# Optimization experiments

Measured on AMD Instinct MI355X. Metric: run time of the kernel, lower is better.

The kernel has to match this reference:

```python
import jax, jax.numpy as jnp
import numpy as np

N_NODES = 100000
N_EDGES = 1600000
D_IN, D_HID, D_OUT = 128, 64, 16


def _glorot(key, shape):
    lim = float(np.sqrt(6.0 / (shape[0] + shape[1])))
    return jax.random.uniform(key, shape, jnp.float32, -lim, lim)


def setup_inputs() -> dict:
    key = jax.random.key(0)
    k1, k2, k3 = jax.random.split(key, 3)
    x = jax.random.normal(k1, (N_NODES, D_IN), dtype=jnp.float32)
    edge_index = jax.random.randint(k2, (2, N_EDGES), 0, N_NODES, dtype=jnp.int64)
    kw1, kw2 = jax.random.split(k3)
    W1 = _glorot(kw1, (D_IN, D_HID))
    b1 = jnp.zeros((D_HID,), jnp.float32)
    W2 = _glorot(kw2, (D_HID, D_OUT))
    b2 = jnp.zeros((D_OUT,), jnp.float32)
    return {"x": x, "edge_index": edge_index, "W1": W1, "b1": b1, "W2": W2, "b2": b2}


def _gcn_conv(h, W, b, src, dst, norm, n_nodes):
    # PyG GCNConv: linear first, then normalized neighbor aggregation, then bias.
    h = h @ W                                        # [N, d_out]
    msg = h[src] * norm[:, None]                     # gather over edges(+self loops)
    out = jax.ops.segment_sum(msg, dst, num_segments=n_nodes)  # scatter-add
    return out + b


def reference(x, edge_index, W1, b1, W2, b2):
    n = x.shape[0]
    loop = jnp.arange(n, dtype=edge_index.dtype)
    src = jnp.concatenate([edge_index[0], loop])     # add self loops
    dst = jnp.concatenate([edge_index[1], loop])
    # symmetric normalization D^-1/2 (A+I) D^-1/2
    deg = jax.ops.segment_sum(jnp.ones(src.shape[0], x.dtype), dst, num_segments=n)
    dinv = jnp.where(deg > 0, jax.lax.rsqrt(jnp.maximum(deg, 1e-12)), 0.0)
    norm = dinv[src] * dinv[dst]                     # [E+N]

    out = _gcn_conv(x, W1, b1, src, dst, norm, n)
    out = jax.nn.sigmoid(out)
    # dropout p=0.5 with training=False -> identity (eval mode)
    out = _gcn_conv(out, W2, b2, src, dst, norm, n)
    return jax.nn.log_softmax(out, axis=1)
```

## Files before the change

kernel.cpp:

```cpp
#include <hip/hip_runtime.h>
#include <hip/hip_bf16.h>


constexpr int D_IN  = 128;
constexpr int D_HID = 64;
constexpr int D_OUT = 16;

constexpr int WSHIFT  = 9;
constexpr int MAXB    = 256;
constexpr int BCAP    = 12288;
constexpr int CSRCAP  = 16384;
constexpr int BIN_CAP = 48;
constexpr int CHUNK   = 4096;

typedef __attribute__((ext_vector_type(8))) short bf16x8;
typedef __attribute__((ext_vector_type(4))) float f32x4;
typedef __attribute__((ext_vector_type(2))) float f32x2;

__device__ inline float bflo(unsigned u){ return __uint_as_float(u << 16); }
__device__ inline float bfhi(unsigned u){ return __uint_as_float(u & 0xffff0000u); }
__device__ inline unsigned f2bu(float f){
    __hip_bfloat16 h = __float2bfloat16(f);
    return (unsigned)*reinterpret_cast<unsigned short*>(&h);
}
__device__ inline float sigf(float x){ return 1.0f / (1.0f + __expf(-x)); }

__global__ __launch_bounds__(256) void k_bucketize(
    const int* __restrict__ ei, const unsigned* __restrict__ xraw,
    int* __restrict__ flags, unsigned* __restrict__ gcur,
    unsigned* __restrict__ gbuf, int ne, int B)
{
    __shared__ unsigned bcnt[MAXB];
    __shared__ unsigned bbase[MAXB];
    __shared__ unsigned bins[MAXB * BIN_CAP];
    __shared__ int s_i64;

    const int t = threadIdx.x, lane = t & 63, wv = t >> 6;
    const int e0 = blockIdx.x * CHUNK;

    if (t < MAXB) bcnt[t] = 0u;
    if (wv == 0){
        int w = ei[2 * lane + 1];
        unsigned long long m = __ballot(w == 0);
        if (lane == 0) s_i64 = (__popcll(m) > 48) ? 1 : 0;
        if (blockIdx.x == 0){
            unsigned u = xraw[lane];
            unsigned h0 = u & 0xffffu, h1 = u >> 16;
            unsigned ex0 = (h0 >> 7) & 0xffu, ex1 = (h1 >> 7) & 0xffu;
            bool bad0 = !((h0 & 0x7fffu) == 0 || (ex0 >= 97 && ex0 <= 157));
            bool bad1 = !((h1 & 0x7fffu) == 0 || (ex1 >= 97 && ex1 <= 157));
            unsigned long long m0 = __ballot(bad0);
            unsigned long long m1 = __ballot(bad1);
            if (lane == 0){
                int bad = __popcll(m0) + __popcll(m1);
                flags[0] = (bad > 8) ? 0 : 1;
                flags[1] = s_i64;
            }
        }
    }
    __syncthreads();
    const int i64 = s_i64;
    const bool vec = ((ne & 1) == 0);

    #pragma unroll
    for (int k = 0; k < CHUNK / 512; ++k){
        int e = e0 + k * 512 + 2 * t;
        int s0, d0, s1, d1;
        int cntE = 0;
        if (vec && e < ne){
            if (i64){
                int4 sp = *(const int4*)&ei[2 * e];
                int4 dp = *(const int4*)&ei[2 * (ne + e)];
                s0 = sp.x; s1 = sp.z; d0 = dp.x; d1 = dp.z;
            } else {
                int2 sp = *(const int2*)&ei[e];
                int2 dp = *(const int2*)&ei[ne + e];
                s0 = sp.x; s1 = sp.y; d0 = dp.x; d1 = dp.y;
            }
            cntE = 2;
        } else {
            if (e < ne){
                if (i64){ s0 = ei[2*e]; d0 = ei[2*(ne+e)]; }
                else    { s0 = ei[e];   d0 = ei[ne+e]; }
                cntE = 1;
                if (e + 1 < ne){
                    if (i64){ s1 = ei[2*(e+1)]; d1 = ei[2*(ne+e+1)]; }
                    else    { s1 = ei[e+1];     d1 = ei[ne+e+1]; }
                    cntE = 2;
                }
            }
        }
        #pragma unroll
        for (int j = 0; j < 2; ++j){
            if (j < cntE){
                int s = j ? s1 : s0, d = j ? d1 : d0;
                int b = d >> WSHIFT;
                unsigned v = ((unsigned)s << WSHIFT) | ((unsigned)d & ((1u << WSHIFT) - 1));
                unsigned p = atomicAdd(&bcnt[b], 1u);
                if (p < (unsigned)BIN_CAP){
                    bins[b * BIN_CAP + p] = v;
                } else {
                    unsigned g = atomicAdd(&gcur[b], 1u);
                    gbuf[(size_t)b * BCAP + g] = v;
                }
            }
        }
    }
    __syncthreads();

    if (t < B){
        unsigned c = min(bcnt[t], (unsigned)BIN_CAP);
        bbase[t] = atomicAdd(&gcur[t], c);
    }
    __syncthreads();

    for (int b = wv; b < B; b += 4){
        unsigned c = min(bcnt[b], (unsigned)BIN_CAP);
        unsigned ba = bbase[b];
        for (unsigned o = lane; o < c; o += 64)
            gbuf[(size_t)b * BCAP + ba + o] = bins[b * BIN_CAP + o];
    }
}

__global__ __launch_bounds__(1024) void k_build(
    const unsigned* __restrict__ gbuf, const unsigned* __restrict__ gcnt,
    unsigned* __restrict__ off, unsigned* __restrict__ offend,
    float* __restrict__ dinv, int* __restrict__ csr, int n, int B)
{
    __shared__ unsigned hist[512];
    __shared__ unsigned offl[512];
    __shared__ unsigned wsums[8];

    const int t = threadIdx.x, lane = t & 63, wv = t >> 6;
    const int b = blockIdx.x;
    const int base = b << WSHIFT;
    const int nodes = min(512, n - base);
    const unsigned bb = (unsigned)b * CSRCAP;

    if (t < 512) hist[t] = 0u;
    __syncthreads();
    const unsigned cnt = gcnt[b];
    const unsigned* mybuf = gbuf + (size_t)b * BCAP;

    for (unsigned i = t; i < cnt; i += 1024)
        atomicAdd(&hist[mybuf[i] & ((1u << WSHIFT) - 1)], 1u);
    __syncthreads();

    unsigned v = 0, p = 0, x = 0;
    if (t < 512){
        v = hist[t];
        p = (v + 7u) & ~7u;
        x = p;
        #pragma unroll
        for (int o = 1; o < 64; o <<= 1){
            unsigned y = __shfl_up(x, o, 64);
            if (lane >= o) x += y;
        }
        if (lane == 63) wsums[wv] = x;
    }
    __syncthreads();
    if (t == 0){
        unsigned run = 0;
        #pragma unroll
        for (int w = 0; w < 8; ++w){ unsigned tv = wsums[w]; wsums[w] = run; run += tv; }
    }
    __syncthreads();
    if (t < 512) offl[t] = x - p + wsums[wv];
    __syncthreads();

    if (t < nodes){
        off[base + t]    = bb + offl[t];
        offend[base + t] = bb + offl[t] + p;
        dinv[base + t]   = rsqrtf(1.0f + (float)v);
    }
    __syncthreads();

    if (t < 512) hist[t] = offl[t];
    __syncthreads();

    for (unsigned i = t; i < cnt; i += 1024){
        unsigned rec = mybuf[i];
        unsigned pos = atomicAdd(&hist[rec & ((1u << WSHIFT) - 1)], 1u);
        csr[bb + pos] = (int)(rec >> WSHIFT);
    }
    __syncthreads();

    if (t < nodes){
        unsigned s = offl[t] + v, e2 = offl[t] + p;
        for (unsigned j = s; j < e2; ++j) csr[bb + j] = n;
    }
}

__global__ __launch_bounds__(256) void k_linear1(
    const unsigned* __restrict__ xraw, const unsigned* __restrict__ w1raw,
    const int* __restrict__ flags, const float* __restrict__ dinv,
    unsigned char* __restrict__ h1f, int n)
{
    const int lane = threadIdx.x & 63;
    const int wv   = threadIdx.x >> 6;
    const int m = lane & 15, q = lane >> 4;
    const int isBf16 = flags[0];

    if (blockIdx.x == 0 && threadIdx.x < 16)
        ((unsigned*)(h1f + (size_t)n * 64))[threadIdx.x] = 0u;

    bf16x8 bfr[4][4];
    if (isBf16){
        const unsigned short* w = (const unsigned short*)w1raw;
        #pragma unroll
        for (int kc = 0; kc < 4; ++kc)
            #pragma unroll
            for (int ct = 0; ct < 4; ++ct)
                #pragma unroll
                for (int j = 0; j < 8; ++j)
                    bfr[kc][ct][j] = (short)w[(kc*32 + q*8 + j) * D_HID + ct*16 + m];
    } else {
        const float* w = (const float*)w1raw;
        #pragma unroll
        for (int kc = 0; kc < 4; ++kc)
            #pragma unroll
            for (int ct = 0; ct < 4; ++ct)
                #pragma unroll
                for (int j = 0; j < 8; ++j)
                    bfr[kc][ct][j] = (short)f2bu(w[(kc*32 + q*8 + j) * D_HID + ct*16 + m]);
    }

    const int ntiles = (n + 15) >> 4;
    for (int tile = blockIdx.x * 4 + wv; tile < ntiles; tile += gridDim.x * 4){
        const int node0 = tile << 4;
        int arow = node0 + m; if (arow >= n) arow = n - 1;
        f32x4 ac0 = {0,0,0,0}, ac1 = {0,0,0,0}, ac2 = {0,0,0,0}, ac3 = {0,0,0,0};
        #pragma unroll
        for (int kc = 0; kc < 4; ++kc){
            bf16x8 a;
            if (isBf16){
                uint4 u = *(const uint4*)((const unsigned short*)xraw + (size_t)arow * D_IN + kc*32 + q*8);
                a = *reinterpret_cast<bf16x8*>(&u);
            } else {
                const float* xp = (const float*)xraw + (size_t)arow * D_IN + kc*32 + q*8;
                float4 f0 = *(const float4*)xp;
                float4 f1 = *(const float4*)(xp + 4);
                a[0]=(short)f2bu(f0.x); a[1]=(short)f2bu(f0.y); a[2]=(short)f2bu(f0.z); a[3]=(short)f2bu(f0.w);
                a[4]=(short)f2bu(f1.x); a[5]=(short)f2bu(f1.y); a[6]=(short)f2bu(f1.z); a[7]=(short)f2bu(f1.w);
            }
            ac0 = __builtin_amdgcn_mfma_f32_16x16x32_bf16(a, bfr[kc][0], ac0, 0, 0, 0);
            ac1 = __builtin_amdgcn_mfma_f32_16x16x32_bf16(a, bfr[kc][1], ac1, 0, 0, 0);
            ac2 = __builtin_amdgcn_mfma_f32_16x16x32_bf16(a, bfr[kc][2], ac2, 0, 0, 0);
            ac3 = __builtin_amdgcn_mfma_f32_16x16x32_bf16(a, bfr[kc][3], ac3, 0, 0, 0);
        }
        #pragma unroll
        for (int i = 0; i < 4; ++i){
            int nr = node0 + q*4 + i;
            if (nr < n){
                float di = dinv[nr];
                int lo = __builtin_amdgcn_cvt_pk_fp8_f32(ac0[i] * di, ac1[i] * di, 0, false);
                int w4 = __builtin_amdgcn_cvt_pk_fp8_f32(ac2[i] * di, ac3[i] * di, lo, true);
                *(unsigned*)(h1f + (size_t)nr * 64 + m * 4) = (unsigned)w4;
            }
        }
    }
}

__global__ __launch_bounds__(256) void k_aggA(
    const unsigned* __restrict__ off, const unsigned* __restrict__ offend,
    const int* __restrict__ csr_src,
    const float* __restrict__ dinv, const unsigned char* __restrict__ h1f,
    const unsigned* __restrict__ b1raw, const unsigned* __restrict__ w2raw,
    const int* __restrict__ flags,
    unsigned short* __restrict__ h2s, int n)
{
    __shared__ unsigned short act_s[16][72];

    const int lane = threadIdx.x & 63;
    const int wv   = threadIdx.x >> 6;
    const int grp  = lane >> 4;
    const int f    = lane & 15;
    const int dl   = wv * 4 + grp;
    const int d    = blockIdx.x * 16 + dl;
    const int isBf16 = flags[0];

    bf16x8 w2f[2];
    if (wv == 0){
        const int m0 = lane & 15, q0 = lane >> 4;
        if (isBf16){
            const unsigned short* w = (const unsigned short*)w2raw;
            #pragma unroll
            for (int kc = 0; kc < 2; ++kc)
                #pragma unroll
                for (int j = 0; j < 8; ++j)
                    w2f[kc][j] = (short)w[(kc*32 + q0*8 + j) * D_OUT + m0];
        } else {
            const float* w = (const float*)w2raw;
            #pragma unroll
            for (int kc = 0; kc < 2; ++kc)
                #pragma unroll
                for (int j = 0; j < 8; ++j)
                    w2f[kc][j] = (short)f2bu(w[(kc*32 + q0*8 + j) * D_OUT + m0]);
        }
        if (blockIdx.x == 0 && lane < 4)
            ((uint2*)(h2s + (size_t)n * D_OUT))[lane] = make_uint2(0u, 0u);
    }

    if (d < n){
        const int beg = (int)off[d], end = (int)offend[d];
        float a0=0.f, a1=0.f, a2=0.f, a3=0.f;
        for (int i = beg; i < end; i += 8){
            uint4 cA = *(const uint4*)&csr_src[i];
            uint4 cB = *(const uint4*)&csr_src[i + 4];
            unsigned u0 = *(const unsigned*)&h1f[(size_t)(unsigned)cA.x * 64 + f * 4];
            unsigned u1 = *(const unsigned*)&h1f[(size_t)(unsigned)cA.y * 64 + f * 4];
            unsigned u2 = *(const unsigned*)&h1f[(size_t)(unsigned)cA.z * 64 + f * 4];
            unsigned u3 = *(const unsigned*)&h1f[(size_t)(unsigned)cA.w * 64 + f * 4];
            unsigned u4 = *(const unsigned*)&h1f[(size_t)(unsigned)cB.x * 64 + f * 4];
            unsigned u5 = *(const unsigned*)&h1f[(size_t)(unsigned)cB.y * 64 + f * 4];
            unsigned u6 = *(const unsigned*)&h1f[(size_t)(unsigned)cB.z * 64 + f * 4];
            unsigned u7 = *(const unsigned*)&h1f[(size_t)(unsigned)cB.w * 64 + f * 4];
            #pragma unroll
            for (int r = 0; r < 8; ++r){
                unsigned uu = r==0?u0: r==1?u1: r==2?u2: r==3?u3: r==4?u4: r==5?u5: r==6?u6: u7;
                f32x2 p01 = __builtin_amdgcn_cvt_pk_f32_fp8((int)uu, false);
                f32x2 p23 = __builtin_amdgcn_cvt_pk_f32_fp8((int)uu, true);
                a0 += p01.x; a1 += p01.y; a2 += p23.x; a3 += p23.y;
            }
        }
        {
            unsigned su = *(const unsigned*)&h1f[(size_t)d * 64 + f * 4];
            f32x2 p01 = __builtin_amdgcn_cvt_pk_f32_fp8((int)su, false);
            f32x2 p23 = __builtin_amdgcn_cvt_pk_f32_fp8((int)su, true);
            a0 += p01.x; a1 += p01.y; a2 += p23.x; a3 += p23.y;
        }
        const float dd = dinv[d];
        float b0, b1v, b2v, b3v;
        if (isBf16){
            const unsigned short* bs = (const unsigned short*)b1raw;
            b0  = bflo(bs[f]);      b1v = bflo(bs[f + 16]);
            b2v = bflo(bs[f + 32]); b3v = bflo(bs[f + 48]);
        } else {
            const float* bs = (const float*)b1raw;
            b0 = bs[f]; b1v = bs[f + 16]; b2v = bs[f + 32]; b3v = bs[f + 48];
        }
        act_s[dl][f]      = (unsigned short)f2bu(sigf(fmaf(a0, dd, b0)));
        act_s[dl][f + 16] = (unsigned short)f2bu(sigf(fmaf(a1, dd, b1v)));
        act_s[dl][f + 32] = (unsigned short)f2bu(sigf(fmaf(a2, dd, b2v)));
        act_s[dl][f + 48] = (unsigned short)f2bu(sigf(fmaf(a3, dd, b3v)));
    } else {
        act_s[dl][f] = 0; act_s[dl][f + 16] = 0;
        act_s[dl][f + 32] = 0; act_s[dl][f + 48] = 0;
    }
    __syncthreads();

    if (wv == 0){
        const int m0 = lane & 15, q0 = lane >> 4;
        f32x4 acc = {0,0,0,0};
        #pragma unroll
        for (int kc = 0; kc < 2; ++kc){
            bf16x8 a;
            #pragma unroll
            for (int j = 0; j < 8; ++j)
                a[j] = (short)act_s[m0][kc*32 + q0*8 + j];
            acc = __builtin_amdgcn_mfma_f32_16x16x32_bf16(a, w2f[kc], acc, 0, 0, 0);
        }
        #pragma unroll
        for (int i = 0; i < 4; ++i){
            int nr = blockIdx.x * 16 + q0*4 + i;
            if (nr < n)
                h2s[(size_t)nr * D_OUT + m0] = (unsigned short)f2bu(acc[i] * dinv[nr]);
        }
    }
}

__global__ __launch_bounds__(256) void k_aggB(
    const unsigned* __restrict__ off, const unsigned* __restrict__ offend,
    const int* __restrict__ csr_src,
    const float* __restrict__ dinv, const unsigned short* __restrict__ h2s,
    const unsigned* __restrict__ b2raw, const int* __restrict__ flags,
    void* __restrict__ out, int n)
{
    const int lane = threadIdx.x & 63;
    const int wv   = threadIdx.x >> 6;
    const int grp  = lane >> 2;
    const int f    = lane & 3;
    const int d    = (blockIdx.x * 4 + wv) * 16 + grp;
    const int isBf16 = flags[0];
    if (d >= n) return;

    const int beg = (int)off[d], end = (int)offend[d];
    float a0=0.f, a1=0.f, a2=0.f, a3=0.f;
    for (int i = beg; i < end; i += 8){
        uint4 cA = *(const uint4*)&csr_src[i];
        uint4 cB = *(const uint4*)&csr_src[i + 4];
        uint2 u0 = *(const uint2*)&h2s[(size_t)(unsigned)cA.x * D_OUT + f * 4];
        uint2 u1 = *(const uint2*)&h2s[(size_t)(unsigned)cA.y * D_OUT + f * 4];
        uint2 u2 = *(const uint2*)&h2s[(size_t)(unsigned)cA.z * D_OUT + f * 4];
        uint2 u3 = *(const uint2*)&h2s[(size_t)(unsigned)cA.w * D_OUT + f * 4];
        uint2 u4 = *(const uint2*)&h2s[(size_t)(unsigned)cB.x * D_OUT + f * 4];
        uint2 u5 = *(const uint2*)&h2s[(size_t)(unsigned)cB.y * D_OUT + f * 4];
        uint2 u6 = *(const uint2*)&h2s[(size_t)(unsigned)cB.z * D_OUT + f * 4];
        uint2 u7 = *(const uint2*)&h2s[(size_t)(unsigned)cB.w * D_OUT + f * 4];
        a0 += bflo(u0.x) + bflo(u1.x) + bflo(u2.x) + bflo(u3.x)
            + bflo(u4.x) + bflo(u5.x) + bflo(u6.x) + bflo(u7.x);
        a1 += bfhi(u0.x) + bfhi(u1.x) + bfhi(u2.x) + bfhi(u3.x)
            + bfhi(u4.x) + bfhi(u5.x) + bfhi(u6.x) + bfhi(u7.x);
        a2 += bflo(u0.y) + bflo(u1.y) + bflo(u2.y) + bflo(u3.y)
            + bflo(u4.y) + bflo(u5.y) + bflo(u6.y) + bflo(u7.y);
        a3 += bfhi(u0.y) + bfhi(u1.y) + bfhi(u2.y) + bfhi(u3.y)
            + bfhi(u4.y) + bfhi(u5.y) + bfhi(u6.y) + bfhi(u7.y);
    }
    uint2 su = *(const uint2*)&h2s[(size_t)d * D_OUT + f * 4];
    a0 += bflo(su.x); a1 += bfhi(su.x);
    a2 += bflo(su.y); a3 += bfhi(su.y);
    const float dd = dinv[d];
    float b0, b1v, b2v, b3v;
    if (isBf16){
        uint2 bu = ((const uint2*)b2raw)[f];
        b0 = bflo(bu.x); b1v = bfhi(bu.x); b2v = bflo(bu.y); b3v = bfhi(bu.y);
    } else {
        float4 bb = ((const float4*)b2raw)[f];
        b0 = bb.x; b1v = bb.y; b2v = bb.z; b3v = bb.w;
    }
    a0 = fmaf(a0, dd, b0); a1 = fmaf(a1, dd, b1v);
    a2 = fmaf(a2, dd, b2v); a3 = fmaf(a3, dd, b3v);
    float m = fmaxf(fmaxf(a0, a1), fmaxf(a2, a3));
    m = fmaxf(m, __shfl_xor(m, 1, 4));
    m = fmaxf(m, __shfl_xor(m, 2, 4));
    float s = __expf(a0 - m) + __expf(a1 - m) + __expf(a2 - m) + __expf(a3 - m);
    s += __shfl_xor(s, 1, 4);
    s += __shfl_xor(s, 2, 4);
    float ls = m + __logf(s);
    if (isBf16){
        uint2 pk;
        pk.x = f2bu(a0 - ls) | (f2bu(a1 - ls) << 16);
        pk.y = f2bu(a2 - ls) | (f2bu(a3 - ls) << 16);
        *(uint2*)((__hip_bfloat16*)out + (size_t)d * D_OUT + f * 4) = pk;
    } else {
        float4 o4 = make_float4(a0 - ls, a1 - ls, a2 - ls, a3 - ls);
        *(float4*)((float*)out + (size_t)d * D_OUT + f * 4) = o4;
    }
}

extern "C" void kernel_launch(void* const* d_in, const int* in_sizes, int n_in,
                              void* d_out, int out_size, void* d_ws, size_t ws_size,
                              hipStream_t stream)
{
    const unsigned* xraw  = (const unsigned*)d_in[0];
    const int*      ei    = (const int*)d_in[1];
    const unsigned* w1raw = (const unsigned*)d_in[2];
    const unsigned* b1raw = (const unsigned*)d_in[3];
    const unsigned* w2raw = (const unsigned*)d_in[4];
    const unsigned* b2raw = (const unsigned*)d_in[5];

    const int n  = in_sizes[0] / D_IN;
    const int ne = in_sizes[1] / 2;
    const int B  = (n + ((1 << WSHIFT) - 1)) >> WSHIFT;

    size_t nAl = ((size_t)n + 255) & ~(size_t)255;
    int*            flags  = (int*)d_ws;
    unsigned*       gcur   = (unsigned*)d_ws + 64;
    float*          dinv   = (float*)(gcur + 256);
    unsigned*       off    = (unsigned*)(dinv + nAl);
    unsigned*       offend = off + nAl;
    int*            csr    = (int*)(offend + nAl);
    unsigned*       gbuf   = (unsigned*)(csr + (size_t)MAXB * CSRCAP);
    unsigned char*  h1f    = (unsigned char*)(gbuf + (size_t)MAXB * BCAP);
    unsigned short* h2s    = (unsigned short*)(h1f + (size_t)(n + 16) * 64);

    const int nchunk  = (ne + CHUNK - 1) / CHUNK;
    const int ntiles1 = (n + 15) / 16;
    const int grid1   = (ntiles1 + 3) / 4;

    hipMemsetAsync(gcur, 0, MAXB * sizeof(unsigned), stream);
    k_bucketize <<<nchunk, 256, 0, stream>>>(ei, xraw, flags, gcur, gbuf, ne, B);
    k_build     <<<B, 1024, 0, stream>>>(gbuf, gcur, off, offend, dinv, csr, n, B);

    k_linear1   <<<grid1, 256, 0, stream>>>(xraw, w1raw, flags, dinv, h1f, n);
    k_aggA      <<<(n + 15) / 16, 256, 0, stream>>>(off, offend, csr, dinv, h1f, b1raw, w2raw, flags, h2s, n);
    k_aggB      <<<(n + 63) / 64, 256, 0, stream>>>(off, offend, csr, dinv, h2s, b2raw, flags, d_out, n);
}
```

Measured before the change: 188.8 us.

## Gather 16-byte fp8 rows with 4 lanes per node in layer-1 aggregation

The layer-1 aggregation kernel now assigns 4 lanes per destination node, each loading a 16-byte slice of the fp8 row, instead of 16 lanes each loading 4 bytes. Each block handles 64 nodes, and every wave runs its own 16-row MFMA for the second linear layer rather than only wave 0. This cuts gather instruction count, raises nodes per wave, and spreads the MFMA epilogue across all waves. The cost is more accumulator registers per lane and a different feature-to-lane mapping for bias and LDS writes.

```diff
diff --git a/kernel.cpp b/kernel.cpp
--- a/kernel.cpp
+++ b/kernel.cpp
@@ -269,103 +269,114 @@
     const int* __restrict__ flags,
     unsigned short* __restrict__ h2s, int n)
 {
-    __shared__ unsigned short act_s[16][72];
+    __shared__ unsigned short act_s[64][72];
 
     const int lane = threadIdx.x & 63;
     const int wv   = threadIdx.x >> 6;
-    const int grp  = lane >> 4;
-    const int f    = lane & 15;
-    const int dl   = wv * 4 + grp;
-    const int d    = blockIdx.x * 16 + dl;
+    const int grp  = lane >> 2;
+    const int f    = lane & 3;
+    const int dl   = wv * 16 + grp;
+    const int d    = blockIdx.x * 64 + dl;
     const int isBf16 = flags[0];
+    const int m0 = lane & 15, q0 = lane >> 4;
 
     bf16x8 w2f[2];
-    if (wv == 0){
-        const int m0 = lane & 15, q0 = lane >> 4;
-        if (isBf16){
-            const unsigned short* w = (const unsigned short*)w2raw;
-            #pragma unroll
-            for (int kc = 0; kc < 2; ++kc)
-                #pragma unroll
-                for (int j = 0; j < 8; ++j)
-                    w2f[kc][j] = (short)w[(kc*32 + q0*8 + j) * D_OUT + m0];
-        } else {
-            const float* w = (const float*)w2raw;
-            #pragma unroll
-            for (int kc = 0; kc < 2; ++kc)
-                #pragma unroll
-                for (int j = 0; j < 8; ++j)
-                    w2f[kc][j] = (short)f2bu(w[(kc*32 + q0*8 + j) * D_OUT + m0]);
-        }
-        if (blockIdx.x == 0 && lane < 4)
-            ((uint2*)(h2s + (size_t)n * D_OUT))[lane] = make_uint2(0u, 0u);
-    }
+    if (isBf16){
+        const unsigned short* w = (const unsigned short*)w2raw;
+        #pragma unroll
+        for (int kc = 0; kc < 2; ++kc)
+            #pragma unroll
+            for (int j = 0; j < 8; ++j)
+                w2f[kc][j] = (short)w[(kc*32 + q0*8 + j) * D_OUT + m0];
+    } else {
+        const float* w = (const float*)w2raw;
+        #pragma unroll
+        for (int kc = 0; kc < 2; ++kc)
+            #pragma unroll
+            for (int j = 0; j < 8; ++j)
+                w2f[kc][j] = (short)f2bu(w[(kc*32 + q0*8 + j) * D_OUT + m0]);
+    }
+    if (blockIdx.x == 0 && threadIdx.x < 4)
+        ((uint2*)(h2s + (size_t)n * D_OUT))[threadIdx.x] = make_uint2(0u, 0u);
 
     if (d < n){
         const int beg = (int)off[d], end = (int)offend[d];
-        float a0=0.f, a1=0.f, a2=0.f, a3=0.f;
+        float a[4][4];
+        #pragma unroll
+        for (int k = 0; k < 4; ++k)
+            #pragma unroll
+            for (int j = 0; j < 4; ++j) a[k][j] = 0.f;
+
         for (int i = beg; i < end; i += 8){
             uint4 cA = *(const uint4*)&csr_src[i];
             uint4 cB = *(const uint4*)&csr_src[i + 4];
-            unsigned u0 = *(const unsigned*)&h1f[(size_t)(unsigned)cA.x * 64 + f * 4];
-            unsigned u1 = *(const unsigned*)&h1f[(size_t)(unsigned)cA.y * 64 + f * 4];
-            unsigned u2 = *(const unsigned*)&h1f[(size_t)(unsigned)cA.z * 64 + f * 4];
-            unsigned u3 = *(const unsigned*)&h1f[(size_t)(unsigned)cA.w * 64 + f * 4];
-            unsigned u4 = *(const unsigned*)&h1f[(size_t)(unsigned)cB.x * 64 + f * 4];
-            unsigned u5 = *(const unsigned*)&h1f[(size_t)(unsigned)cB.y * 64 + f * 4];
-            unsigned u6 = *(const unsigned*)&h1f[(size_t)(unsigned)cB.z * 64 + f * 4];
-            unsigned u7 = *(const unsigned*)&h1f[(size_t)(unsigned)cB.w * 64 + f * 4];
+            uint4 g0 = *(const uint4*)&h1f[(size_t)(unsigned)cA.x * 64 + f * 16];
+            uint4 g1 = *(const uint4*)&h1f[(size_t)(unsigned)cA.y * 64 + f * 16];
+            uint4 g2 = *(const uint4*)&h1f[(size_t)(unsigned)cA.z * 64 + f * 16];
+            uint4 g3 = *(const uint4*)&h1f[(size_t)(unsigned)cA.w * 64 + f * 16];
+            uint4 g4 = *(const uint4*)&h1f[(size_t)(unsigned)cB.x * 64 + f * 16];
+            uint4 g5 = *(const uint4*)&h1f[(size_t)(unsigned)cB.y * 64 + f * 16];
+            uint4 g6 = *(const uint4*)&h1f[(size_t)(unsigned)cB.z * 64 + f * 16];
+            uint4 g7 = *(const uint4*)&h1f[(size_t)(unsigned)cB.w * 64 + f * 16];
             #pragma unroll
             for (int r = 0; r < 8; ++r){
-                unsigned uu = r==0?u0: r==1?u1: r==2?u2: r==3?u3: r==4?u4: r==5?u5: r==6?u6: u7;
-                f32x2 p01 = __builtin_amdgcn_cvt_pk_f32_fp8((int)uu, false);
-                f32x2 p23 = __builtin_amdgcn_cvt_pk_f32_fp8((int)uu, true);
-                a0 += p01.x; a1 += p01.y; a2 += p23.x; a3 += p23.y;
+                uint4 g = r==0?g0: r==1?g1: r==2?g2: r==3?g3: r==4?g4: r==5?g5: r==6?g6: g7;
+                #pragma unroll
+                for (int j = 0; j < 4; ++j){
+                    unsigned dw = j==0?g.x: j==1?g.y: j==2?g.z: g.w;
+                    f32x2 p01 = __builtin_amdgcn_cvt_pk_f32_fp8((int)dw, false);
+                    f32x2 p23 = __builtin_amdgcn_cvt_pk_f32_fp8((int)dw, true);
+                    a[0][j] += p01.x; a[1][j] += p01.y;
+                    a[2][j] += p23.x; a[3][j] += p23.y;
+                }
             }
         }
         {
-            unsigned su = *(const unsigned*)&h1f[(size_t)d * 64 + f * 4];
-            f32x2 p01 = __builtin_amdgcn_cvt_pk_f32_fp8((int)su, false);
-            f32x2 p23 = __builtin_amdgcn_cvt_pk_f32_fp8((int)su, true);
-            a0 += p01.x; a1 += p01.y; a2 += p23.x; a3 += p23.y;
+            uint4 g = *(const uint4*)&h1f[(size_t)d * 64 + f * 16];
+            #pragma unroll
+            for (int j = 0; j < 4; ++j){
+                unsigned dw = j==0?g.x: j==1?g.y: j==2?g.z: g.w;
+                f32x2 p01 = __builtin_amdgcn_cvt_pk_f32_fp8((int)dw, false);
+                f32x2 p23 = __builtin_amdgcn_cvt_pk_f32_fp8((int)dw, true);
+                a[0][j] += p01.x; a[1][j] += p01.y;
+                a[2][j] += p23.x; a[3][j] += p23.y;
+            }
         }
         const float dd = dinv[d];
-        float b0, b1v, b2v, b3v;
-        if (isBf16){
-            const unsigned short* bs = (const unsigned short*)b1raw;
-            b0  = bflo(bs[f]);      b1v = bflo(bs[f + 16]);
-            b2v = bflo(bs[f + 32]); b3v = bflo(bs[f + 48]);
-        } else {
-            const float* bs = (const float*)b1raw;
-            b0 = bs[f]; b1v = bs[f + 16]; b2v = bs[f + 32]; b3v = bs[f + 48];
-        }
-        act_s[dl][f]      = (unsigned short)f2bu(sigf(fmaf(a0, dd, b0)));
-        act_s[dl][f + 16] = (unsigned short)f2bu(sigf(fmaf(a1, dd, b1v)));
-        act_s[dl][f + 32] = (unsigned short)f2bu(sigf(fmaf(a2, dd, b2v)));
-        act_s[dl][f + 48] = (unsigned short)f2bu(sigf(fmaf(a3, dd, b3v)));
+        #pragma unroll
+        for (int k = 0; k < 4; ++k){
+            #pragma unroll
+            for (int j = 0; j < 4; ++j){
+                const int feat = k*16 + 4*f + j;
+                float bv;
+                if (isBf16) bv = bflo(((const unsigned short*)b1raw)[feat]);
+                else        bv = ((const float*)b1raw)[feat];
+                act_s[dl][feat] = (unsigned short)f2bu(sigf(fmaf(a[k][j], dd, bv)));
+            }
+        }
     } else {
-        act_s[dl][f] = 0; act_s[dl][f + 16] = 0;
-        act_s[dl][f + 32] = 0; act_s[dl][f + 48] = 0;
-    }
-    __syncthreads();
-
-    if (wv == 0){
-        const int m0 = lane & 15, q0 = lane >> 4;
-        f32x4 acc = {0,0,0,0};
-        #pragma unroll
-        for (int kc = 0; kc < 2; ++kc){
-            bf16x8 a;
-            #pragma unroll
-            for (int j = 0; j < 8; ++j)
-                a[j] = (short)act_s[m0][kc*32 + q0*8 + j];
-            acc = __builtin_amdgcn_mfma_f32_16x16x32_bf16(a, w2f[kc], acc, 0, 0, 0);
-        }
-        #pragma unroll
-        for (int i = 0; i < 4; ++i){
-            int nr = blockIdx.x * 16 + q0*4 + i;
-            if (nr < n)
-                h2s[(size_t)nr * D_OUT + m0] = (unsigned short)f2bu(acc[i] * dinv[nr]);
-        }
+        #pragma unroll
+        for (int k = 0; k < 4; ++k)
+            #pragma unroll
+            for (int j = 0; j < 4; ++j)
+                act_s[dl][k*16 + 4*f + j] = 0;
+    }
+    __syncthreads();
+
+    f32x4 acc = {0,0,0,0};
+    #pragma unroll
+    for (int kc = 0; kc < 2; ++kc){
+        bf16x8 av;
+        #pragma unroll
+        for (int j = 0; j < 8; ++j)
+            av[j] = (short)act_s[wv*16 + m0][kc*32 + q0*8 + j];
+        acc = __builtin_amdgcn_mfma_f32_16x16x32_bf16(av, w2f[kc], acc, 0, 0, 0);
+    }
+    #pragma unroll
+    for (int i = 0; i < 4; ++i){
+        int nr = blockIdx.x * 64 + wv*16 + q0*4 + i;
+        if (nr < n)
+            h2s[(size_t)nr * D_OUT + m0] = (unsigned short)f2bu(acc[i] * dinv[nr]);
     }
 }
 
@@ -473,6 +484,6 @@
     k_build     <<<B, 1024, 0, stream>>>(gbuf, gcur, off, offend, dinv, csr, n, B);
 
     k_linear1   <<<grid1, 256, 0, stream>>>(xraw, w1raw, flags, dinv, h1f, n);
-    k_aggA      <<<(n + 15) / 16, 256, 0, stream>>>(off, offend, csr, dinv, h1f, b1raw, w2raw, flags, h2s, n);
+    k_aggA      <<<(n + 63) / 64, 256, 0, stream>>>(off, offend, csr, dinv, h1f, b1raw, w2raw, flags, h2s, n);
     k_aggB      <<<(n + 63) / 64, 256, 0, stream>>>(off, offend, csr, dinv, h2s, b2raw, flags, d_out, n);
 }
```

New measurement: 197.6 us. +4.7%, slower.
